# Kernel tuning notes

Hardware: AMD Instinct MI355X
Metric: run time of the kernel (lower is better)

Reference implementation:

```python
import jax, jax.numpy as jnp
import numpy as np


def setup_inputs() -> dict:
    key = jax.random.key(0)
    kq, kk, kv = jax.random.split(key, 3)
    B, H, N, D = 2, 16, 2048, 64
    q = jax.random.normal(kq, (B, H, N, D), dtype=jnp.float32)
    k = jax.random.normal(kk, (B, H, N, D), dtype=jnp.float32)
    v = jax.random.normal(kv, (B, H, N, D), dtype=jnp.float32)
    return {"q": q, "k": k, "v": v}


def reference(q, k, v):
    # RBF-kernel causal attention: logits = -relu(||q-k||^2) / sqrt(D)
    B, H, N, D = q.shape
    sm_scale = 1.0 / jnp.sqrt(jnp.asarray(D, dtype=q.dtype))
    q_sq = jnp.sum(q * q, axis=-1)              # [B,H,N]
    k_sq = jnp.sum(k * k, axis=-1)              # [B,H,N]
    qk = jnp.einsum("bhmd,bhnd->bhmn", q, k)    # [B,H,N,N]
    dist_sq = q_sq[..., :, None] + k_sq[..., None, :] - 2.0 * qk
    dist_sq = jnp.maximum(dist_sq, 0.0)         # relu on squared distance
    logits = -dist_sq * sm_scale
    # causal mask: query m attends to keys n <= m
    causal = jnp.tril(jnp.ones((N, N), dtype=bool))
    logits = jnp.where(causal, logits, -jnp.inf)
    p = jax.nn.softmax(logits, axis=-1)
    out = jnp.einsum("bhmn,bhnd->bhmd", p, v)
    return out
```

## Files before the change

### kernel.cpp

```cpp
#include <hip/hip_runtime.h>

#define NN 2048
#define DD 64
#define C1 0.36067376f
#define C1H 0.18033688f

typedef _Float16 h8 __attribute__((ext_vector_type(8)));
typedef _Float16 h4 __attribute__((ext_vector_type(4)));
typedef float f32x16 __attribute__((ext_vector_type(16)));

union H8U4 { h8 v; unsigned u[4]; };

__global__ __launch_bounds__(64) void prep(const float* __restrict__ k,
                                           const float* __restrict__ v,
                                           _Float16* __restrict__ Ks,
                                           _Float16* __restrict__ Vs,
                                           float* __restrict__ hk) {
    __shared__ _Float16 T[32][72];
    const int jj = blockIdx.x, bh = blockIdx.y, lane = threadIdx.x;
    const int ln = lane & 31, lh = lane >> 5;
    const size_t ibase = (size_t)bh * NN * DD + (size_t)jj * 32 * DD;

    {
        const float* kr = k + ibase + (size_t)ln * DD;
        float s = 0.f;
#pragma unroll
        for (int c = 0; c < 4; ++c) {
            float4 a = *(const float4*)&kr[16 * c + 8 * lh];
            float4 b = *(const float4*)&kr[16 * c + 8 * lh + 4];
            h8 o = {(_Float16)a.x, (_Float16)a.y, (_Float16)a.z, (_Float16)a.w,
                    (_Float16)b.x, (_Float16)b.y, (_Float16)b.z, (_Float16)b.w};
            *(h8*)&Ks[((size_t)bh * 16384 + jj * 256 + c * 64 + lh * 32 + ln) * 8] = o;
            s += a.x*a.x + a.y*a.y + a.z*a.z + a.w*a.w
               + b.x*b.x + b.y*b.y + b.z*b.z + b.w*b.w;
        }
        s += __shfl_xor(s, 32);
        if (lh == 0) hk[bh * NN + jj * 32 + ln] = s * C1H;
    }

#pragma unroll
    for (int t = 0; t < 8; ++t) {
        int f = lane + 64 * t;
        int row = f >> 4, c4 = (f & 15) * 4;
        float4 a = *(const float4*)&v[ibase + (size_t)row * DD + c4];
        h4 hv = {(_Float16)a.x, (_Float16)a.y, (_Float16)a.z, (_Float16)a.w};
        *(h4*)&T[row][c4] = hv;
    }
    __syncthreads();
#pragma unroll
    for (int oc = 0; oc < 4; ++oc) {
        int o = oc >> 1, c = oc & 1;
        h8 r;
#pragma unroll
        for (int jx = 0; jx < 8; ++jx) r[jx] = T[16 * c + 8 * lh + jx][32 * o + ln];
        *(h8*)&Vs[((size_t)bh * 16384 + jj * 256 + o * 128 + c * 64 + lh * 32 + ln) * 8] = r;
    }
}

__global__ __launch_bounds__(128, 2) void rbf_attn(
    const float* __restrict__ q, const _Float16* __restrict__ Ks,
    const _Float16* __restrict__ Vs, const float* __restrict__ hk,
    float* __restrict__ out)
{
    const int tid = threadIdx.x;
    const int bh = blockIdx.x;
    const int qb = 31 - blockIdx.y;
    const int wv = tid >> 6, lane = tid & 63;
    const int ln = lane & 31, lh = lane >> 5;
    const int jmax = 2 * qb + wv;
    const int qrow = qb * 64 + wv * 32 + ln;
    const size_t fbase = (size_t)bh * NN * DD;

    h8 qf[4];
    {
        const float* qr = q + fbase + (size_t)qrow * DD;
#pragma unroll
        for (int c = 0; c < 4; ++c) {
            float4 a = *(const float4*)&qr[16 * c + 8 * lh];
            float4 b = *(const float4*)&qr[16 * c + 8 * lh + 4];
            qf[c] = h8{(_Float16)a.x, (_Float16)a.y, (_Float16)a.z, (_Float16)a.w,
                       (_Float16)b.x, (_Float16)b.y, (_Float16)b.z, (_Float16)b.w};
        }
    }

    const _Float16* Ksb = Ks + (size_t)bh * 131072;
    const _Float16* Vsb = Vs + (size_t)bh * 131072;
    const float4* hk4 = (const float4*)(hk + bh * NN);
    const int klq = (lh * 32 + ln) * 8;

    f32x16 O0, O1;
#pragma unroll
    for (int r = 0; r < 16; ++r) { O0[r] = 0.f; O1[r] = 0.f; }
    float lsum = 0.f, mrun = -INFINITY;

    auto loadT = [&](int jj, h8 (&kf)[4], h8 (&vf)[4], float4 (&hr)[4]) {
        const _Float16* kp = Ksb + (size_t)jj * 2048 + klq;
        const _Float16* vp = Vsb + (size_t)jj * 2048 + klq;
#pragma unroll
        for (int c = 0; c < 4; ++c) kf[c] = *(const h8*)(kp + c * 512);
#pragma unroll
        for (int oc = 0; oc < 4; ++oc)
            vf[oc] = *(const h8*)(vp + (oc >> 1) * 1024 + (oc & 1) * 512);
#pragma unroll
        for (int g = 0; g < 4; ++g) hr[g] = hk4[jj * 8 + g * 2 + lh];
    };

    auto comp = [&](int jj, h8 (&kf)[4], h8 (&vf)[4], float4 (&hr)[4]) {
        f32x16 S;
#pragma unroll
        for (int r = 0; r < 16; ++r) S[r] = 0.f;
#pragma unroll
        for (int c = 0; c < 4; ++c)
            S = __builtin_amdgcn_mfma_f32_32x32x16_f16(kf[c], qf[c], S, 0, 0, 0);

        const bool diag = (jj == jmax);
        float x[16];
#pragma unroll
        for (int r = 0; r < 16; ++r) {
            const float* hf = (const float*)&hr[r >> 2];
            float xv = fmaf(S[r], C1, -hf[r & 3]);
            if (diag) {
                int keyloc = (r & 3) + 8 * (r >> 2) + 4 * lh;
                if (keyloc > ln) xv = -INFINITY;
            }
            x[r] = xv;
        }
        float mt = x[0];
#pragma unroll
        for (int r = 1; r < 16; ++r) mt = fmaxf(mt, x[r]);
        mt = fmaxf(mt, __shfl_xor(mt, 32));
        float mnew = fmaxf(mrun, mt);
        float alpha = __builtin_amdgcn_exp2f(mrun - mnew);
        mrun = mnew;
        float p[16], ps = 0.f;
#pragma unroll
        for (int r = 0; r < 16; ++r) {
            p[r] = __builtin_amdgcn_exp2f(x[r] - mnew);
            ps += p[r];
        }
        lsum = fmaf(lsum, alpha, ps);
#pragma unroll
        for (int r = 0; r < 16; ++r) { O0[r] *= alpha; O1[r] *= alpha; }

        unsigned pk[8];
#pragma unroll
        for (int hh = 0; hh < 8; ++hh) {
            auto pr = __builtin_amdgcn_cvt_pkrtz(p[2 * hh], p[2 * hh + 1]);
            unsigned pu; __builtin_memcpy(&pu, &pr, 4);
            pk[hh] = pu;
        }
#pragma unroll
        for (int s = 0; s < 2; ++s) {
            unsigned send0 = lh ? pk[4 * s + 0] : pk[4 * s + 2];
            unsigned send1 = lh ? pk[4 * s + 1] : pk[4 * s + 3];
            unsigned r0 = (unsigned)__shfl_xor((int)send0, 32);
            unsigned r1 = (unsigned)__shfl_xor((int)send1, 32);
            H8U4 pb;
            pb.u[0] = lh ? r0 : pk[4 * s + 0];
            pb.u[1] = lh ? r1 : pk[4 * s + 1];
            pb.u[2] = lh ? pk[4 * s + 2] : r0;
            pb.u[3] = lh ? pk[4 * s + 3] : r1;
            O0 = __builtin_amdgcn_mfma_f32_32x32x16_f16(vf[s], pb.v, O0, 0, 0, 0);
            O1 = __builtin_amdgcn_mfma_f32_32x32x16_f16(vf[2 + s], pb.v, O1, 0, 0, 0);
        }
    };

    h8 kfA[4], vfA[4]; float4 hrA[4];
    h8 kfB[4], vfB[4]; float4 hrB[4];
    loadT(0, kfA, vfA, hrA);
    int jj = 0;
    while (true) {
        if (jj < jmax) loadT(jj + 1, kfB, vfB, hrB);
        comp(jj, kfA, vfA, hrA);
        if (++jj > jmax) break;
        if (jj < jmax) loadT(jj + 1, kfA, vfA, hrA);
        comp(jj, kfB, vfB, hrB);
        if (++jj > jmax) break;
    }

    float lt = lsum + __shfl_xor(lsum, 32);
    float inv = 1.f / lt;
    size_t ro = fbase + (size_t)qrow * DD;
#pragma unroll
    for (int g = 0; g < 4; ++g) {
        float4 o0 = make_float4(O0[4 * g + 0] * inv, O0[4 * g + 1] * inv,
                                O0[4 * g + 2] * inv, O0[4 * g + 3] * inv);
        *(float4*)&out[ro + 8 * g + 4 * lh] = o0;
        float4 o1 = make_float4(O1[4 * g + 0] * inv, O1[4 * g + 1] * inv,
                                O1[4 * g + 2] * inv, O1[4 * g + 3] * inv);
        *(float4*)&out[ro + 32 + 8 * g + 4 * lh] = o1;
    }
}

extern "C" void kernel_launch(void* const* d_in, const int* in_sizes, int n_in,
                              void* d_out, int out_size, void* d_ws, size_t ws_size,
                              hipStream_t stream) {
    (void)in_sizes; (void)n_in; (void)out_size; (void)ws_size;
    const float* q = (const float*)d_in[0];
    const float* k = (const float*)d_in[1];
    const float* v = (const float*)d_in[2];
    float* out = (float*)d_out;

    float* hk = (float*)d_ws;
    _Float16* Ks = (_Float16*)((char*)d_ws + 262144);
    _Float16* Vs = (_Float16*)((char*)d_ws + 262144 + 8388608);

    prep<<<dim3(64, 32), 64, 0, stream>>>(k, v, Ks, Vs, hk);
    rbf_attn<<<dim3(32, 32), 128, 0, stream>>>(q, Ks, Vs, hk, out);
}
```

Measured before the change: 137.1 us.

## Enlarge prep blocks, skip redundant rescale, pin load/compute schedule

The prep kernel now handles 128 keys per 256-thread block and stages K through shared memory for coalesced loads, with row norms reduced by 16-lane shuffles. The attention loop rescales O and lsum only when some lane's running max rises, detected with a wave ballot, which skips the multiplies on most tiles. Scheduling barriers are placed between the prefetch loads and the compute so the compiler keeps the software pipeline order. The ballot adds a branch, and the barriers may block useful instruction interleaving.

```diff
diff --git a/kernel.cpp b/kernel.cpp
--- a/kernel.cpp
+++ b/kernel.cpp
@@ -11,36 +11,45 @@
 
 union H8U4 { h8 v; unsigned u[4]; };
 
-__global__ __launch_bounds__(64) void prep(const float* __restrict__ k,
-                                           const float* __restrict__ v,
-                                           _Float16* __restrict__ Ks,
-                                           _Float16* __restrict__ Vs,
-                                           float* __restrict__ hk) {
-    __shared__ _Float16 T[32][72];
-    const int jj = blockIdx.x, bh = blockIdx.y, lane = threadIdx.x;
-    const int ln = lane & 31, lh = lane >> 5;
-    const size_t ibase = (size_t)bh * NN * DD + (size_t)jj * 32 * DD;
-
-    {
-        const float* kr = k + ibase + (size_t)ln * DD;
-        float s = 0.f;
-#pragma unroll
-        for (int c = 0; c < 4; ++c) {
-            float4 a = *(const float4*)&kr[16 * c + 8 * lh];
-            float4 b = *(const float4*)&kr[16 * c + 8 * lh + 4];
-            h8 o = {(_Float16)a.x, (_Float16)a.y, (_Float16)a.z, (_Float16)a.w,
-                    (_Float16)b.x, (_Float16)b.y, (_Float16)b.z, (_Float16)b.w};
-            *(h8*)&Ks[((size_t)bh * 16384 + jj * 256 + c * 64 + lh * 32 + ln) * 8] = o;
-            s += a.x*a.x + a.y*a.y + a.z*a.z + a.w*a.w
-               + b.x*b.x + b.y*b.y + b.z*b.z + b.w*b.w;
-        }
-        s += __shfl_xor(s, 32);
-        if (lh == 0) hk[bh * NN + jj * 32 + ln] = s * C1H;
-    }
-
-#pragma unroll
-    for (int t = 0; t < 8; ++t) {
-        int f = lane + 64 * t;
+__global__ __launch_bounds__(256) void prep(const float* __restrict__ k,
+                                            const float* __restrict__ v,
+                                            _Float16* __restrict__ Ks,
+                                            _Float16* __restrict__ Vs,
+                                            float* __restrict__ hk) {
+    __shared__ _Float16 T[128][72];
+    const int tb = blockIdx.x, bh = blockIdx.y, tid = threadIdx.x;
+    const size_t ibase = (size_t)bh * NN * DD + (size_t)tb * 128 * DD;
+    const int lane = tid & 63, ln = lane & 31, lh = lane >> 5;
+
+#pragma unroll
+    for (int it = 0; it < 8; ++it) {
+        int f = tid + 256 * it;
+        int row = f >> 4, c4 = (f & 15) * 4;
+        float4 a = *(const float4*)&k[ibase + (size_t)row * DD + c4];
+        h4 hv = {(_Float16)a.x, (_Float16)a.y, (_Float16)a.z, (_Float16)a.w};
+        *(h4*)&T[row][c4] = hv;
+        float s = a.x * a.x + a.y * a.y + a.z * a.z + a.w * a.w;
+        s += __shfl_xor(s, 1, 16);
+        s += __shfl_xor(s, 2, 16);
+        s += __shfl_xor(s, 4, 16);
+        s += __shfl_xor(s, 8, 16);
+        if ((tid & 15) == 0) hk[bh * NN + tb * 128 + row] = s * C1H;
+    }
+    __syncthreads();
+#pragma unroll
+    for (int it = 0; it < 4; ++it) {
+        int f2 = tid + 256 * it;
+        int combo = f2 >> 6;
+        int jl = combo >> 2, c = combo & 3;
+        h8 r = *(const h8*)&T[32 * jl + ln][16 * c + 8 * lh];
+        *(h8*)&Ks[(size_t)bh * 131072 + (size_t)(4 * tb + jl) * 2048
+                  + (size_t)(c * 64 + lane) * 8] = r;
+    }
+    __syncthreads();
+
+#pragma unroll
+    for (int it = 0; it < 8; ++it) {
+        int f = tid + 256 * it;
         int row = f >> 4, c4 = (f & 15) * 4;
         float4 a = *(const float4*)&v[ibase + (size_t)row * DD + c4];
         h4 hv = {(_Float16)a.x, (_Float16)a.y, (_Float16)a.z, (_Float16)a.w};
@@ -48,12 +57,16 @@
     }
     __syncthreads();
 #pragma unroll
-    for (int oc = 0; oc < 4; ++oc) {
-        int o = oc >> 1, c = oc & 1;
+    for (int it = 0; it < 4; ++it) {
+        int f2 = tid + 256 * it;
+        int combo = f2 >> 6;
+        int jl = combo >> 2, o = (combo >> 1) & 1, c = combo & 1;
         h8 r;
 #pragma unroll
-        for (int jx = 0; jx < 8; ++jx) r[jx] = T[16 * c + 8 * lh + jx][32 * o + ln];
-        *(h8*)&Vs[((size_t)bh * 16384 + jj * 256 + o * 128 + c * 64 + lh * 32 + ln) * 8] = r;
+        for (int jx = 0; jx < 8; ++jx)
+            r[jx] = T[32 * jl + 16 * c + 8 * lh + jx][32 * o + ln];
+        *(h8*)&Vs[(size_t)bh * 131072 + (size_t)(4 * tb + jl) * 2048
+                  + (size_t)(o * 128 + c * 64 + lane) * 8] = r;
     }
 }
 
@@ -129,18 +142,21 @@
 #pragma unroll
         for (int r = 1; r < 16; ++r) mt = fmaxf(mt, x[r]);
         mt = fmaxf(mt, __shfl_xor(mt, 32));
-        float mnew = fmaxf(mrun, mt);
-        float alpha = __builtin_amdgcn_exp2f(mrun - mnew);
-        mrun = mnew;
+        if (__ballot(mt > mrun) != 0ull) {
+            float mnew = fmaxf(mrun, mt);
+            float alpha = __builtin_amdgcn_exp2f(mrun - mnew);
+            mrun = mnew;
+            lsum *= alpha;
+#pragma unroll
+            for (int r = 0; r < 16; ++r) { O0[r] *= alpha; O1[r] *= alpha; }
+        }
         float p[16], ps = 0.f;
 #pragma unroll
         for (int r = 0; r < 16; ++r) {
-            p[r] = __builtin_amdgcn_exp2f(x[r] - mnew);
+            p[r] = __builtin_amdgcn_exp2f(x[r] - mrun);
             ps += p[r];
         }
-        lsum = fmaf(lsum, alpha, ps);
-#pragma unroll
-        for (int r = 0; r < 16; ++r) { O0[r] *= alpha; O1[r] *= alpha; }
+        lsum += ps;
 
         unsigned pk[8];
 #pragma unroll
@@ -168,13 +184,18 @@
     h8 kfA[4], vfA[4]; float4 hrA[4];
     h8 kfB[4], vfB[4]; float4 hrB[4];
     loadT(0, kfA, vfA, hrA);
+    __builtin_amdgcn_sched_barrier(0);
     int jj = 0;
     while (true) {
         if (jj < jmax) loadT(jj + 1, kfB, vfB, hrB);
+        __builtin_amdgcn_sched_barrier(0);
         comp(jj, kfA, vfA, hrA);
+        __builtin_amdgcn_sched_barrier(0);
         if (++jj > jmax) break;
         if (jj < jmax) loadT(jj + 1, kfA, vfA, hrA);
+        __builtin_amdgcn_sched_barrier(0);
         comp(jj, kfB, vfB, hrB);
+        __builtin_amdgcn_sched_barrier(0);
         if (++jj > jmax) break;
     }
 
@@ -205,6 +226,6 @@
     _Float16* Ks = (_Float16*)((char*)d_ws + 262144);
     _Float16* Vs = (_Float16*)((char*)d_ws + 262144 + 8388608);
 
-    prep<<<dim3(64, 32), 64, 0, stream>>>(k, v, Ks, Vs, hk);
+    prep<<<dim3(16, 32), 256, 0, stream>>>(k, v, Ks, Vs, hk);
     rbf_attn<<<dim3(32, 32), 128, 0, stream>>>(q, Ks, Vs, hk, out);
 }
```

Result: no change. 138.4 us (+0.9%).
